# Performance work log

Hardware: AMD Instinct MI355X
Metric: run time of the kernel (lower is better)

## Reference

```python
import jax, jax.numpy as jnp
import numpy as np

NC = 10   # num_classes
H = 6     # num_heads
C = 384   # dim
HD = C // H
B = 16    # batch (non-anchor rows)
T = 197   # tokens (1 cls + 196 image)
N = T - 1
SCALE = HD ** -0.5


def _ln(x, g, b):
    mu = jnp.mean(x, -1, keepdims=True)
    var = jnp.mean(jnp.square(x - mu), -1, keepdims=True)
    return (x - mu) * jax.lax.rsqrt(var + 1e-5) * g + b


def setup_inputs() -> dict:
    key = jax.random.key(0)
    ks = jax.random.split(key, 12)
    def w(k, shape):
        return jax.random.normal(k, shape, jnp.float32) * 0.02
    return {
        "x": jax.random.normal(ks[0], (B + NC, T, C), jnp.float32),
        "Wqv": w(ks[1], (C, 2 * C)),
        "Wk": w(ks[2], (C, C)),
        "Wq_proj": w(ks[3], (C, C)), "bq_proj": jnp.zeros((C,), jnp.float32),
        "Wqk": w(ks[4], (C, C)), "Wqk2": w(ks[5], (C, C)), "Wv": w(ks[6], (C, C)),
        "Wr_proj": w(ks[7], (C, C)), "br_proj": jnp.zeros((C,), jnp.float32),
        "g1": jnp.ones((C,), jnp.float32), "b1": jnp.zeros((C,), jnp.float32),
        "g2": jnp.ones((C,), jnp.float32), "b2": jnp.zeros((C,), jnp.float32),
        "g3": jnp.ones((C,), jnp.float32), "b3": jnp.zeros((C,), jnp.float32),
        "W1": w(ks[8], (C, 4 * C)), "bm1": jnp.zeros((4 * C,), jnp.float32),
        "W2": w(ks[9], (4 * C, C)), "bm2": jnp.zeros((C,), jnp.float32),
    }


def reference(x, Wqv, Wk, Wq_proj, bq_proj, Wqk, Wqk2, Wv, Wr_proj, br_proj,
              g1, b1, g2, b2, g3, b3, W1, bm1, W2, bm2):
    xs, anchors = x[:-NC], jax.lax.stop_gradient(x[-NC:])  # anchors .detach()
    x_im, a_im = xs[:, 1:], anchors[:, 1:]                  # [B,N,C], [NC,N,C]
    x_cls, a_cls = xs[:, :1], anchors[:, :1]                # [B,1,C], [NC,1,C]

    # ---- Quoter ----
    n1x = _ln(x_cls, g1, b1)[:, 0]    # [B,C]
    n1a = _ln(a_cls, g1, b1)[:, 0]    # [NC,C]
    qv = (n1a @ Wqv).reshape(NC, 2, H, HD)
    q, v = qv[:, 0], qv[:, 1]                       # [NC,H,HD]
    k = (n1x @ Wk).reshape(B, H, HD)                # [B,H,HD]
    attn_cls = jax.nn.softmax(jnp.einsum('nhd,bhd->bnh', q, k) * SCALE, axis=1)  # [B,NC,H]
    cls_out = jnp.einsum('bnh,nhd->bhd', attn_cls, v).reshape(B, 1, C) @ Wq_proj + bq_proj

    # ---- Rectifier ----
    n2x = _ln(x_im, g2, b2)   # [B,N,C]
    n2a = _ln(a_im, g2, b2)   # [NC,N,C]
    def heads(t, W):
        return (t @ W).reshape(t.shape[0], N, H, HD).transpose(0, 2, 1, 3)
    vr = heads(n2x, Wv)        # [B,H,N,HD]
    qh = heads(n2x, Wqk)       # [B,H,N,HD]
    kh = heads(n2a, Wqk)       # [NC,H,N,HD]
    q2 = heads(n2x, Wqk2)
    k2 = heads(n2a, Wqk2)
    # left_attn = relu(-(q @ k^T) * scale), right_attn = relu((k2 @ q2^T) * scale)
    left = jax.nn.relu(-SCALE * jnp.einsum('bhnd,chmd->bchnm', qh, kh))    # [B,NC,H,N,N]
    right = jax.nn.relu(SCALE * jnp.einsum('chmd,bhnd->bchmn', k2, q2))    # [B,NC,H,N,N]
    attn = jnp.einsum('bchnm,bchmk->bchnk', left, right).transpose(0, 2, 3, 1, 4)  # [B,H,N,NC,N]
    # faithful raw reshape [B,NC,H] -> [B,H,NC] (memory reinterpretation as in torch source)
    w2 = attn_cls.reshape(B, H, NC)
    tmp = jnp.einsum('bhc,bhnck->bhnk', w2, attn)                           # [B,H,N,N]
    # faithful raw reshape [B,H,N,HD] -> [B,N,C]
    rect = jnp.einsum('bhnk,bhkd->bhnd', tmp, vr).reshape(B, N, C) @ Wr_proj + br_proj

    x_im = x_im + rect
    xx = jnp.concatenate([cls_out, x_im], axis=1)        # [B,T,C]
    hdn = _ln(xx, g3, b3)
    xx = xx + (jax.nn.gelu(hdn @ W1 + bm1, approximate=False) @ W2 + bm2)
    return jnp.concatenate([xx, anchors], axis=0)        # [B+NC,T,C]
```

## Files before the change

### kernel.cpp

```cpp
#include <hip/hip_runtime.h>
#include <hip/hip_bf16.h>
#include <math.h>

#define SCL 0.125f

typedef float f32x4 __attribute__((ext_vector_type(4)));
typedef short bf16x8 __attribute__((ext_vector_type(8)));
#define MFMA16(a, b, c) __builtin_amdgcn_mfma_f32_16x16x32_bf16((a), (b), (c), 0, 0, 0)

__device__ __forceinline__ unsigned short f2bf(float f) {
    unsigned int u = __builtin_bit_cast(unsigned int, f);
    u = (u + 0x7FFFu + ((u >> 16) & 1u)) >> 16;
    return (unsigned short)u;
}

__device__ __forceinline__ float gelu_exact(float v) {
    return 0.5f * v * (1.f + erff(v * 0.70710678118654752f));
}

template <int BF16OUT>
__global__ void ln_kernel(const float* __restrict__ x, void* __restrict__ outp,
                          const float* __restrict__ g, const float* __restrict__ bt,
                          int mode) {
    const int row = blockIdx.x;
    const int lane = threadIdx.x;
    const float* src;
    if (mode == 0)      src = x + (size_t)row * (197 * 384);
    else if (mode == 1) { int b = row / 196, n = row % 196; src = x + (size_t)(b * 197 + 1 + n) * 384; }
    else if (mode == 2) { int b = row / 196, n = row % 196; src = x + (size_t)((16 + b) * 197 + 1 + n) * 384; }
    else                src = x + (size_t)row * 384;

    float v[6];
    float s = 0.f, s2 = 0.f;
#pragma unroll
    for (int j = 0; j < 6; j++) {
        v[j] = src[lane + j * 64];
        s += v[j];
        s2 += v[j] * v[j];
    }
#pragma unroll
    for (int o = 32; o; o >>= 1) {
        s  += __shfl_xor(s, o);
        s2 += __shfl_xor(s2, o);
    }
    const float mu = s * (1.f / 384.f);
    const float var = s2 * (1.f / 384.f) - mu * mu;
    const float rs = 1.f / sqrtf(var + 1e-5f);
#pragma unroll
    for (int j = 0; j < 6; j++) {
        const int c = lane + j * 64;
        const float r = (v[j] - mu) * rs * g[c] + bt[c];
        if (BF16OUT) ((unsigned short*)outp)[(size_t)row * 384 + c] = f2bf(r);
        else         ((float*)outp)[(size_t)row * 384 + c] = r;
    }
}

template <int M>
__global__ void gemm_cls(const float* __restrict__ A, const float* __restrict__ B,
                         const float* __restrict__ bias, float* __restrict__ C,
                         int N, int ldc) {
    __shared__ float sA[M * 384];
    __shared__ float red[4][M][64];
    const int t = threadIdx.x;
    const int tc = t & 63, ks = t >> 6;
    const int n = blockIdx.x * 64 + tc;
    for (int e = t; e < M * 384; e += 256) sA[e] = A[e];
    __syncthreads();
    float acc[M];
#pragma unroll
    for (int m = 0; m < M; m++) acc[m] = 0.f;
    const int k0 = ks * 96;
#pragma unroll 4
    for (int k = k0; k < k0 + 96; k++) {
        const float bv = B[(size_t)k * N + n];
#pragma unroll
        for (int m = 0; m < M; m++) acc[m] += sA[m * 384 + k] * bv;
    }
#pragma unroll
    for (int m = 0; m < M; m++) red[ks][m][tc] = acc[m];
    __syncthreads();
    if (ks == 0) {
#pragma unroll
        for (int m = 0; m < M; m++) {
            float s = red[0][m][tc] + red[1][m][tc] + red[2][m][tc] + red[3][m][tc];
            if (bias) s += bias[n];
            C[(size_t)m * ldc + n] = s;
        }
    }
}

__global__ void attn_cls_kernel(const float* __restrict__ qv, const float* __restrict__ kcls,
                                float* __restrict__ aflat, float* __restrict__ cls_pre) {
    const int b = blockIdx.x;
    const int t = threadIdx.x;
    __shared__ float kb[384];
    __shared__ float pl[60];
#pragma unroll
    for (int j = 0; j < 6; j++) kb[t + j * 64] = kcls[b * 384 + t + j * 64];
    __syncthreads();
    if (t < 60) {
        const int n = t / 6, h = t % 6;
        float acc = 0.f;
        for (int d = 0; d < 64; d++) acc += qv[n * 768 + h * 64 + d] * kb[h * 64 + d];
        pl[t] = acc * SCL;
    }
    __syncthreads();
    if (t < 6) {
        float m = -1e30f;
        for (int n = 0; n < 10; n++) m = fmaxf(m, pl[n * 6 + t]);
        float p[10], sum = 0.f;
        for (int n = 0; n < 10; n++) { p[n] = expf(pl[n * 6 + t] - m); sum += p[n]; }
        const float inv = 1.f / sum;
        for (int n = 0; n < 10; n++) {
            const float pr = p[n] * inv;
            pl[n * 6 + t] = pr;
            aflat[b * 60 + n * 6 + t] = pr;
        }
    }
    __syncthreads();
#pragma unroll
    for (int j = 0; j < 6; j++) {
        const int c = t + j * 64;
        const int h = c >> 6;
        float acc = 0.f;
        for (int n = 0; n < 10; n++) acc += pl[n * 6 + h] * qv[n * 768 + 384 + c];
        cls_pre[b * 384 + c] = acc;
    }
}

__global__ void wcast_t(const float* __restrict__ W, unsigned short* __restrict__ Wt,
                        int K, int N) {
    const int n0 = blockIdx.x * 64, k0 = blockIdx.y * 64;
    __shared__ unsigned short sT[64][72];
    const int t = threadIdx.x;
    for (int e = t; e < 4096; e += 256) {
        const int k = e >> 6, n = e & 63;
        sT[n][k] = f2bf(W[(size_t)(k0 + k) * N + n0 + n]);
    }
    __syncthreads();
    for (int e = t; e < 512; e += 256) {
        const int n = e >> 3, ch = e & 7;
        *(uint4*)&Wt[(size_t)(n0 + n) * K + k0 + ch * 8] = *(uint4*)&sT[n][ch * 8];
    }
}

__global__ void wcast3(const float* __restrict__ Wa, const float* __restrict__ Wb,
                       const float* __restrict__ Wc, unsigned short* __restrict__ Wt) {
    const float* W = blockIdx.z == 0 ? Wa : (blockIdx.z == 1 ? Wb : Wc);
    unsigned short* dst = Wt + (size_t)blockIdx.z * 384 * 384;
    const int n0 = blockIdx.x * 64, k0 = blockIdx.y * 64;
    __shared__ unsigned short sT[64][72];
    const int t = threadIdx.x;
    for (int e = t; e < 4096; e += 256) {
        const int k = e >> 6, n = e & 63;
        sT[n][k] = f2bf(W[(size_t)(k0 + k) * 384 + n0 + n]);
    }
    __syncthreads();
    for (int e = t; e < 512; e += 256) {
        const int n = e >> 3, ch = e & 7;
        *(uint4*)&dst[(size_t)(n0 + n) * 384 + k0 + ch * 8] = *(uint4*)&sT[n][ch * 8];
    }
}

template <int EPI>
__launch_bounds__(256)
__global__ void gemm_mfma(const unsigned short* __restrict__ A,
                          const unsigned short* __restrict__ Bt,
                          const float* __restrict__ bias, const float* __restrict__ res,
                          void* __restrict__ Cout, int M, int N, int K) {
    const int m0 = blockIdx.y * 64, n0 = blockIdx.x * 128;
    const int t = threadIdx.x;
    const int w = t >> 6, l = t & 63;
    const int lr = l & 15, lk = l >> 4;
    const int wr = w >> 1, wc = w & 1;

    __shared__ unsigned short sA[64][72];
    __shared__ unsigned short sB[128][72];

    f32x4 acc[2][4];
#pragma unroll
    for (int mi = 0; mi < 2; mi++)
#pragma unroll
        for (int nj = 0; nj < 4; nj++) acc[mi][nj] = (f32x4){0.f, 0.f, 0.f, 0.f};

    for (int k0 = 0; k0 < K; k0 += 64) {
        for (int e = t; e < 512; e += 256) {
            const int r = e >> 3, ch = e & 7;
            uint4 v = make_uint4(0, 0, 0, 0);
            const int row = m0 + r;
            if (row < M) v = *(const uint4*)(A + (size_t)row * K + k0 + ch * 8);
            *(uint4*)&sA[r][ch * 8] = v;
        }
        for (int e = t; e < 1024; e += 256) {
            const int r = e >> 3, ch = e & 7;
            *(uint4*)&sB[r][ch * 8] = *(const uint4*)(Bt + (size_t)(n0 + r) * K + k0 + ch * 8);
        }
        __syncthreads();
#pragma unroll
        for (int kc = 0; kc < 2; kc++) {
            bf16x8 af[2], bfr[4];
#pragma unroll
            for (int mi = 0; mi < 2; mi++)
                af[mi] = *(const bf16x8*)&sA[wr * 32 + mi * 16 + lr][kc * 32 + lk * 8];
#pragma unroll
            for (int nj = 0; nj < 4; nj++)
                bfr[nj] = *(const bf16x8*)&sB[wc * 64 + nj * 16 + lr][kc * 32 + lk * 8];
#pragma unroll
            for (int mi = 0; mi < 2; mi++)
#pragma unroll
                for (int nj = 0; nj < 4; nj++)
                    acc[mi][nj] = MFMA16(af[mi], bfr[nj], acc[mi][nj]);
        }
        __syncthreads();
    }

#pragma unroll
    for (int mi = 0; mi < 2; mi++)
#pragma unroll
        for (int nj = 0; nj < 4; nj++) {
            const int col = n0 + wc * 64 + nj * 16 + lr;
#pragma unroll
            for (int i = 0; i < 4; i++) {
                const int row = m0 + wr * 32 + mi * 16 + lk * 4 + i;
                if (row >= M) continue;
                float v = acc[mi][nj][i];
                if (EPI == 0) {
                    ((unsigned short*)Cout)[(size_t)row * N + col] = f2bf(v);
                } else if (EPI == 1) {
                    const int crow = row + row / 196 + 1;
                    v += bias[col] + res[(size_t)crow * N + col];
                    ((float*)Cout)[(size_t)crow * N + col] = v;
                } else if (EPI == 2) {
                    ((unsigned short*)Cout)[(size_t)row * N + col] = f2bf(gelu_exact(v + bias[col]));
                } else {
                    v += bias[col] + res[(size_t)row * N + col];
                    ((float*)Cout)[(size_t)row * N + col] = v;
                }
            }
        }
}

__global__ __launch_bounds__(256, 1)
void rz_kernel(const unsigned short* __restrict__ Q2b, const unsigned short* __restrict__ K2b,
               const unsigned short* __restrict__ VRb, unsigned short* __restrict__ Zt,
               int sq, int sk, int sv) {
    const int c = blockIdx.x, h = blockIdx.y, b = blockIdx.z;
    const int t = threadIdx.x;
    const int w = t >> 6, l = t & 63;
    const int lr = l & 15;
    const int lk = l >> 4;

    __shared__ unsigned short sm[78208];
    unsigned short* sQ2 = sm;
    unsigned short* sVT = sm;
    unsigned short* sK2 = sm + 14976;
    unsigned short* sR  = sm + 29952;

    const unsigned short* q2src = Q2b + (size_t)(b * 196) * sq + h * 64;
    const unsigned short* k2src = K2b + (size_t)(c * 196) * sk + h * 64;
    for (int e = t; e < 208 * 8; e += 256) {
        const int r = e >> 3, ch = e & 7;
        uint4 v = make_uint4(0, 0, 0, 0);
        if (r < 196) v = *(const uint4*)(q2src + (size_t)r * sq + ch * 8);
        *(uint4*)&sQ2[r * 72 + ch * 8] = v;
    }
    for (int e = t; e < 208 * 8; e += 256) {
        const int r = e >> 3, ch = e & 7;
        uint4 v = make_uint4(0, 0, 0, 0);
        if (r < 196) v = *(const uint4*)(k2src + (size_t)r * sk + ch * 8);
        *(uint4*)&sK2[r * 72 + ch * 8] = v;
    }
    for (int e = t; e < 208 * 16; e += 256) sR[(e >> 4) * 232 + 208 + (e & 15)] = 0;
    __syncthreads();

    for (int tt = w; tt < 169; tt += 4) {
        const int mt = tt / 13, kt = tt % 13;
        f32x4 acc = {0.f, 0.f, 0.f, 0.f};
        bf16x8 a0 = *(const bf16x8*)&sK2[(mt * 16 + lr) * 72 + lk * 8];
        bf16x8 b0 = *(const bf16x8*)&sQ2[(kt * 16 + lr) * 72 + lk * 8];
        acc = MFMA16(a0, b0, acc);
        bf16x8 a1 = *(const bf16x8*)&sK2[(mt * 16 + lr) * 72 + 32 + lk * 8];
        bf16x8 b1 = *(const bf16x8*)&sQ2[(kt * 16 + lr) * 72 + 32 + lk * 8];
        acc = MFMA16(a1, b1, acc);
        const int rrow = mt * 16 + lk * 4, rcol = kt * 16 + lr;
#pragma unroll
        for (int i = 0; i < 4; i++)
            sR[(rrow + i) * 232 + rcol] = f2bf(fmaxf(0.f, SCL * acc[i]));
    }
    __syncthreads();

    const unsigned short* vrsrc = VRb + (size_t)(b * 196) * sv + h * 64;
    for (int e = t; e < 196 * 8; e += 256) {
        const int kk = e >> 3, ch = e & 7;
        uint4 v = *(const uint4*)(vrsrc + (size_t)kk * sv + ch * 8);
        unsigned short vs[8]; *(uint4*)vs = v;
#pragma unroll
        for (int j = 0; j < 8; j++) sVT[(ch * 8 + j) * 232 + kk] = vs[j];
    }
    for (int e = t; e < 64 * 36; e += 256) sVT[(e / 36) * 232 + 196 + (e % 36)] = 0;
    __syncthreads();

    unsigned short* zdst = Zt + ((((size_t)(b * 6 + h)) * 10 + c) * 64) * 208;
    for (int tt = w; tt < 52; tt += 4) {
        const int mt = tt >> 2, dt = tt & 3;
        f32x4 acc = {0.f, 0.f, 0.f, 0.f};
#pragma unroll
        for (int kc = 0; kc < 7; kc++) {
            bf16x8 a = *(const bf16x8*)&sR[(mt * 16 + lr) * 232 + kc * 32 + lk * 8];
            bf16x8 bb = *(const bf16x8*)&sVT[(dt * 16 + lr) * 232 + kc * 32 + lk * 8];
            acc = MFMA16(a, bb, acc);
        }
        unsigned short p[4];
#pragma unroll
        for (int i = 0; i < 4; i++) p[i] = f2bf(acc[i]);
        *(uint2*)&zdst[(size_t)(dt * 16 + lr) * 208 + mt * 16 + lk * 4] = *(uint2*)p;
    }
}

__global__ __launch_bounds__(256)
void yz_kernel(const unsigned short* __restrict__ QHb, const unsigned short* __restrict__ KHb,
               const unsigned short* __restrict__ Zt, const float* __restrict__ aflat,
               unsigned short* __restrict__ rect) {
    const int ns = blockIdx.x, h = blockIdx.y, b = blockIdx.z;
    const int n0 = ns * 49;
    const int t = threadIdx.x;
    const int w = t >> 6, l = t & 63;
    const int lr = l & 15, lk = l >> 4;

    __shared__ unsigned short sKH[112 * 72];
    __shared__ unsigned short sZT[64 * 232];
    __shared__ unsigned short sL[64 * 232];

    for (int e = t; e < 64 * 24; e += 256) {
        sZT[(e / 24) * 232 + 208 + (e % 24)] = 0;
        sL [(e / 24) * 232 + 208 + (e % 24)] = 0;
    }

    bf16x8 qf[2];
    {
        const int rel = w * 16 + lr;
        if (rel < 49) {
            const unsigned short* qsrc = QHb + (size_t)(b * 196 + n0 + rel) * 1152 + h * 64;
            qf[0] = *(const bf16x8*)(qsrc + lk * 8);
            qf[1] = *(const bf16x8*)(qsrc + 32 + lk * 8);
        } else {
            qf[0] = (bf16x8){0, 0, 0, 0, 0, 0, 0, 0};
            qf[1] = (bf16x8){0, 0, 0, 0, 0, 0, 0, 0};
        }
    }

    f32x4 y[4];
#pragma unroll
    for (int i = 0; i < 4; i++) y[i] = (f32x4){0.f, 0.f, 0.f, 0.f};
    __syncthreads();

    for (int c = 0; c < 10; c++) {
        const unsigned short* zsrc = Zt + ((((size_t)(b * 6 + h)) * 10 + c) * 64) * 208;
        for (int e = t; e < 64 * 26; e += 256) {
            const int d = e / 26, mc = e % 26;
            *(uint4*)&sZT[d * 232 + mc * 8] = *(const uint4*)(zsrc + (size_t)d * 208 + mc * 8);
        }
        for (int e = t; e < 112 * 8; e += 256) {
            const int r = e >> 3, ch = e & 7;
            *(uint4*)&sKH[r * 72 + ch * 8] =
                *(const uint4*)(KHb + (size_t)(c * 196 + r) * 768 + h * 64 + ch * 8);
        }
        const float wc = aflat[b * 60 + h * 10 + c];
        __syncthreads();
#pragma unroll
        for (int mt = 0; mt < 7; mt++) {
            f32x4 acc = {0.f, 0.f, 0.f, 0.f};
            bf16x8 b0 = *(const bf16x8*)&sKH[(mt * 16 + lr) * 72 + lk * 8];
            acc = MFMA16(qf[0], b0, acc);
            bf16x8 b1 = *(const bf16x8*)&sKH[(mt * 16 + lr) * 72 + 32 + lk * 8];
            acc = MFMA16(qf[1], b1, acc);
            const int lrow = w * 16 + lk * 4, lcol = mt * 16 + lr;
#pragma unroll
            for (int i = 0; i < 4; i++)
                sL[(lrow + i) * 232 + lcol] = f2bf(wc * fmaxf(0.f, -SCL * acc[i]));
        }
        __syncthreads();
        for (int e = t; e < 96 * 8; e += 256) {
            const int r = e >> 3, ch = e & 7;
            uint4 v = make_uint4(0, 0, 0, 0);
            if (112 + r < 196)
                v = *(const uint4*)(KHb + (size_t)(c * 196 + 112 + r) * 768 + h * 64 + ch * 8);
            *(uint4*)&sKH[r * 72 + ch * 8] = v;
        }
        __syncthreads();
#pragma unroll
        for (int mt = 7; mt < 13; mt++) {
            f32x4 acc = {0.f, 0.f, 0.f, 0.f};
            bf16x8 b0 = *(const bf16x8*)&sKH[((mt - 7) * 16 + lr) * 72 + lk * 8];
            acc = MFMA16(qf[0], b0, acc);
            bf16x8 b1 = *(const bf16x8*)&sKH[((mt - 7) * 16 + lr) * 72 + 32 + lk * 8];
            acc = MFMA16(qf[1], b1, acc);
            const int lrow = w * 16 + lk * 4, lcol = mt * 16 + lr;
#pragma unroll
            for (int i = 0; i < 4; i++)
                sL[(lrow + i) * 232 + lcol] = f2bf(wc * fmaxf(0.f, -SCL * acc[i]));
        }
#pragma unroll
        for (int dt = 0; dt < 4; dt++) {
            f32x4 acc = y[dt];
#pragma unroll
            for (int mc = 0; mc < 7; mc++) {
                bf16x8 a  = *(const bf16x8*)&sL[(w * 16 + lr) * 232 + mc * 32 + lk * 8];
                bf16x8 bb = *(const bf16x8*)&sZT[(dt * 16 + lr) * 232 + mc * 32 + lk * 8];
                acc = MFMA16(a, bb, acc);
            }
            y[dt] = acc;
        }
        __syncthreads();
    }

#pragma unroll
    for (int dt = 0; dt < 4; dt++)
#pragma unroll
        for (int i = 0; i < 4; i++) {
            const int rel = w * 16 + lk * 4 + i;
            if (rel < 49)
                rect[(((size_t)(b * 6 + h)) * 196 + n0 + rel) * 64 + dt * 16 + lr] = f2bf(y[dt][i]);
        }
}

__global__ void copy_anchors(const float* __restrict__ x, float* __restrict__ out) {
    const int e = blockIdx.x * 256 + threadIdx.x;
    if (e < 189120) {
        const int base = 16 * 197 * 384 / 4;
        ((float4*)out)[base + e] = ((const float4*)x)[base + e];
    }
}

extern "C" void kernel_launch(void* const* d_in, const int* in_sizes, int n_in,
                              void* d_out, int out_size, void* d_ws, size_t ws_size,
                              hipStream_t stream) {
    (void)in_sizes; (void)n_in; (void)out_size; (void)ws_size;
    const float* x       = (const float*)d_in[0];
    const float* Wqv     = (const float*)d_in[1];
    const float* Wk      = (const float*)d_in[2];
    const float* Wq_proj = (const float*)d_in[3];
    const float* bq_proj = (const float*)d_in[4];
    const float* Wqk     = (const float*)d_in[5];
    const float* Wqk2    = (const float*)d_in[6];
    const float* Wv      = (const float*)d_in[7];
    const float* Wr_proj = (const float*)d_in[8];
    const float* br_proj = (const float*)d_in[9];
    const float* g1      = (const float*)d_in[10];
    const float* b1      = (const float*)d_in[11];
    const float* g2      = (const float*)d_in[12];
    const float* b2      = (const float*)d_in[13];
    const float* g3      = (const float*)d_in[14];
    const float* b3      = (const float*)d_in[15];
    const float* W1      = (const float*)d_in[16];
    const float* bm1     = (const float*)d_in[17];
    const float* W2      = (const float*)d_in[18];
    const float* bm2     = (const float*)d_in[19];

    float* ws = (float*)d_ws;
    float* n1      = ws;
    float* qv      = ws + 9984;
    float* kcls    = ws + 17664;
    float* aflat   = ws + 23808;
    float* cls_pre = ws + 24768;
    unsigned short* n2x_bf  = (unsigned short*)(ws + 30912);
    unsigned short* n2a_bf  = (unsigned short*)(ws + 633024);
    unsigned short* Px      = (unsigned short*)(ws + 1009344);
    unsigned short* Pa      = (unsigned short*)(ws + 2815680);
    unsigned short* rect_bf = (unsigned short*)(ws + 3568320);
    float* xx               = ws + 4170432;
    unsigned short* Wx_t    = (unsigned short*)(ws + 5380800);
    unsigned short* Wr_t    = (unsigned short*)(ws + 5601984);
    unsigned short* W1_t    = (unsigned short*)(ws + 5675712);
    unsigned short* W2_t    = (unsigned short*)(ws + 5970624);
    unsigned short* Zt      = (unsigned short*)(ws + 6265536);
    unsigned short* hdn_bf  = (unsigned short*)(ws + 6265536);
    unsigned short* G_bf    = (unsigned short*)(ws + 6870720);
    float* outf = (float*)d_out;

    unsigned short* QHb = Px;
    unsigned short* Q2b = Px + 384;
    unsigned short* VRb = Px + 768;
    unsigned short* KHb = Pa;
    unsigned short* K2b = Pa + 384;

    wcast3<<<dim3(6, 6, 3), 256, 0, stream>>>(Wqk, Wqk2, Wv, Wx_t);
    wcast_t<<<dim3(6, 6),  256, 0, stream>>>(Wr_proj, Wr_t, 384, 384);
    wcast_t<<<dim3(24, 6), 256, 0, stream>>>(W1, W1_t, 384, 1536);
    wcast_t<<<dim3(6, 24), 256, 0, stream>>>(W2, W2_t, 1536, 384);
    ln_kernel<0><<<26, 64, 0, stream>>>(x, n1, g1, b1, 0);
    gemm_cls<10><<<12, 256, 0, stream>>>(n1 + 16 * 384, Wqv, nullptr, qv, 768, 768);
    gemm_cls<16><<<6, 256, 0, stream>>>(n1, Wk, nullptr, kcls, 384, 384);
    attn_cls_kernel<<<16, 64, 0, stream>>>(qv, kcls, aflat, cls_pre);
    ln_kernel<1><<<3136, 64, 0, stream>>>(x, n2x_bf, g2, b2, 1);
    ln_kernel<1><<<1960, 64, 0, stream>>>(x, n2a_bf, g2, b2, 2);
    gemm_mfma<0><<<dim3(9, 49), 256, 0, stream>>>(n2x_bf, Wx_t, nullptr, nullptr, Px, 3136, 1152, 384);
    gemm_mfma<0><<<dim3(6, 31), 256, 0, stream>>>(n2a_bf, Wx_t, nullptr, nullptr, Pa, 1960, 768, 384);
    rz_kernel<<<dim3(10, 6, 16), 256, 0, stream>>>(Q2b, K2b, VRb, Zt, 1152, 768, 1152);
    yz_kernel<<<dim3(4, 6, 16), 256, 0, stream>>>(QHb, KHb, Zt, aflat, rect_bf);
    gemm_cls<16><<<6, 256, 0, stream>>>(cls_pre, Wq_proj, bq_proj, xx, 384, 197 * 384);
    gemm_mfma<1><<<dim3(3, 49), 256, 0, stream>>>(rect_bf, Wr_t, br_proj, x, xx, 3136, 384, 384);
    ln_kernel<1><<<3152, 64, 0, stream>>>(xx, hdn_bf, g3, b3, 3);
    gemm_mfma<2><<<dim3(12, 50), 256, 0, stream>>>(hdn_bf, W1_t, bm1, nullptr, G_bf, 3152, 1536, 384);
    gemm_mfma<3><<<dim3(3, 50), 256, 0, stream>>>(G_bf, W2_t, bm2, xx, outf, 3152, 384, 1536);
    copy_anchors<<<739, 256, 0, stream>>>(x, outf);
}
```

Baseline: 503.4 us.

## Restructure rz_kernel to hold Q2 fragments in registers and fuse per-wave strips

rz_kernel now keeps all Q2 MFMA fragments in registers and loads K2 rows directly from global memory. Each wave computes a 16-row strip of relu(K2·Q2ᵀ) into its own LDS buffer and immediately multiplies it by Vᵀ. This shrinks shared memory use enough to allow two blocks per CU and removes the full-tile staging and a barrier. Separately, the two image-token LayerNorm launches (x and anchors) are merged into one launch, which relies on the anchor output buffer sitting directly after the x buffer. The risk is higher register pressure from 26 held fragments.

```diff
diff --git a/kernel.cpp b/kernel.cpp
--- a/kernel.cpp
+++ b/kernel.cpp
@@ -26,8 +26,10 @@
     const int lane = threadIdx.x;
     const float* src;
     if (mode == 0)      src = x + (size_t)row * (197 * 384);
-    else if (mode == 1) { int b = row / 196, n = row % 196; src = x + (size_t)(b * 197 + 1 + n) * 384; }
-    else if (mode == 2) { int b = row / 196, n = row % 196; src = x + (size_t)((16 + b) * 197 + 1 + n) * 384; }
+    else if (mode == 4) {
+        if (row < 3136) { int b = row / 196, n = row % 196; src = x + (size_t)(b * 197 + 1 + n) * 384; }
+        else { int rr = row - 3136; int b = rr / 196, n = rr % 196; src = x + (size_t)((16 + b) * 197 + 1 + n) * 384; }
+    }
     else                src = x + (size_t)row * 384;
 
     float v[6];
@@ -240,54 +242,18 @@
         }
 }
 
-__global__ __launch_bounds__(256, 1)
+__global__ __launch_bounds__(256, 2)
 void rz_kernel(const unsigned short* __restrict__ Q2b, const unsigned short* __restrict__ K2b,
                const unsigned short* __restrict__ VRb, unsigned short* __restrict__ Zt,
                int sq, int sk, int sv) {
     const int c = blockIdx.x, h = blockIdx.y, b = blockIdx.z;
     const int t = threadIdx.x;
     const int w = t >> 6, l = t & 63;
-    const int lr = l & 15;
-    const int lk = l >> 4;
-
-    __shared__ unsigned short sm[78208];
-    unsigned short* sQ2 = sm;
-    unsigned short* sVT = sm;
-    unsigned short* sK2 = sm + 14976;
-    unsigned short* sR  = sm + 29952;
-
-    const unsigned short* q2src = Q2b + (size_t)(b * 196) * sq + h * 64;
-    const unsigned short* k2src = K2b + (size_t)(c * 196) * sk + h * 64;
-    for (int e = t; e < 208 * 8; e += 256) {
-        const int r = e >> 3, ch = e & 7;
-        uint4 v = make_uint4(0, 0, 0, 0);
-        if (r < 196) v = *(const uint4*)(q2src + (size_t)r * sq + ch * 8);
-        *(uint4*)&sQ2[r * 72 + ch * 8] = v;
-    }
-    for (int e = t; e < 208 * 8; e += 256) {
-        const int r = e >> 3, ch = e & 7;
-        uint4 v = make_uint4(0, 0, 0, 0);
-        if (r < 196) v = *(const uint4*)(k2src + (size_t)r * sk + ch * 8);
-        *(uint4*)&sK2[r * 72 + ch * 8] = v;
-    }
-    for (int e = t; e < 208 * 16; e += 256) sR[(e >> 4) * 232 + 208 + (e & 15)] = 0;
-    __syncthreads();
-
-    for (int tt = w; tt < 169; tt += 4) {
-        const int mt = tt / 13, kt = tt % 13;
-        f32x4 acc = {0.f, 0.f, 0.f, 0.f};
-        bf16x8 a0 = *(const bf16x8*)&sK2[(mt * 16 + lr) * 72 + lk * 8];
-        bf16x8 b0 = *(const bf16x8*)&sQ2[(kt * 16 + lr) * 72 + lk * 8];
-        acc = MFMA16(a0, b0, acc);
-        bf16x8 a1 = *(const bf16x8*)&sK2[(mt * 16 + lr) * 72 + 32 + lk * 8];
-        bf16x8 b1 = *(const bf16x8*)&sQ2[(kt * 16 + lr) * 72 + 32 + lk * 8];
-        acc = MFMA16(a1, b1, acc);
-        const int rrow = mt * 16 + lk * 4, rcol = kt * 16 + lr;
-#pragma unroll
-        for (int i = 0; i < 4; i++)
-            sR[(rrow + i) * 232 + rcol] = f2bf(fmaxf(0.f, SCL * acc[i]));
-    }
-    __syncthreads();
+    const int lr = l & 15, lk = l >> 4;
+
+    __shared__ unsigned short sVT[64 * 232];
+    __shared__ unsigned short sR[4 * 16 * 232];
+    unsigned short* sRw = sR + w * (16 * 232);
 
     const unsigned short* vrsrc = VRb + (size_t)(b * 196) * sv + h * 64;
     for (int e = t; e < 196 * 8; e += 256) {
@@ -298,22 +264,61 @@
         for (int j = 0; j < 8; j++) sVT[(ch * 8 + j) * 232 + kk] = vs[j];
     }
     for (int e = t; e < 64 * 36; e += 256) sVT[(e / 36) * 232 + 196 + (e % 36)] = 0;
-    __syncthreads();
-
+    for (int e = l; e < 16 * 24; e += 64) sRw[(e / 24) * 232 + 208 + (e % 24)] = 0;
+
+    bf16x8 qf0[13], qf1[13];
+    const unsigned short* q2src = Q2b + (size_t)(b * 196) * sq + h * 64;
+#pragma unroll
+    for (int kt = 0; kt < 13; kt++) {
+        const int r = kt * 16 + lr;
+        if (r < 196) {
+            const unsigned short* p = q2src + (size_t)r * sq;
+            qf0[kt] = *(const bf16x8*)(p + lk * 8);
+            qf1[kt] = *(const bf16x8*)(p + 32 + lk * 8);
+        } else {
+            qf0[kt] = (bf16x8){0, 0, 0, 0, 0, 0, 0, 0};
+            qf1[kt] = (bf16x8){0, 0, 0, 0, 0, 0, 0, 0};
+        }
+    }
+    __syncthreads();
+
+    const unsigned short* k2src = K2b + (size_t)(c * 196) * sk + h * 64;
     unsigned short* zdst = Zt + ((((size_t)(b * 6 + h)) * 10 + c) * 64) * 208;
-    for (int tt = w; tt < 52; tt += 4) {
-        const int mt = tt >> 2, dt = tt & 3;
-        f32x4 acc = {0.f, 0.f, 0.f, 0.f};
-#pragma unroll
-        for (int kc = 0; kc < 7; kc++) {
-            bf16x8 a = *(const bf16x8*)&sR[(mt * 16 + lr) * 232 + kc * 32 + lk * 8];
-            bf16x8 bb = *(const bf16x8*)&sVT[(dt * 16 + lr) * 232 + kc * 32 + lk * 8];
-            acc = MFMA16(a, bb, acc);
-        }
-        unsigned short p[4];
-#pragma unroll
-        for (int i = 0; i < 4; i++) p[i] = f2bf(acc[i]);
-        *(uint2*)&zdst[(size_t)(dt * 16 + lr) * 208 + mt * 16 + lk * 4] = *(uint2*)p;
+
+    for (int mt = w; mt < 13; mt += 4) {
+        bf16x8 a0, a1;
+        const int ar = mt * 16 + lr;
+        if (ar < 196) {
+            const unsigned short* p = k2src + (size_t)ar * sk;
+            a0 = *(const bf16x8*)(p + lk * 8);
+            a1 = *(const bf16x8*)(p + 32 + lk * 8);
+        } else {
+            a0 = (bf16x8){0, 0, 0, 0, 0, 0, 0, 0};
+            a1 = (bf16x8){0, 0, 0, 0, 0, 0, 0, 0};
+        }
+#pragma unroll
+        for (int kt = 0; kt < 13; kt++) {
+            f32x4 acc = {0.f, 0.f, 0.f, 0.f};
+            acc = MFMA16(a0, qf0[kt], acc);
+            acc = MFMA16(a1, qf1[kt], acc);
+#pragma unroll
+            for (int i = 0; i < 4; i++)
+                sRw[(lk * 4 + i) * 232 + kt * 16 + lr] = f2bf(fmaxf(0.f, SCL * acc[i]));
+        }
+#pragma unroll
+        for (int dt = 0; dt < 4; dt++) {
+            f32x4 acc = {0.f, 0.f, 0.f, 0.f};
+#pragma unroll
+            for (int kc = 0; kc < 7; kc++) {
+                bf16x8 a  = *(const bf16x8*)&sRw[lr * 232 + kc * 32 + lk * 8];
+                bf16x8 bb = *(const bf16x8*)&sVT[(dt * 16 + lr) * 232 + kc * 32 + lk * 8];
+                acc = MFMA16(a, bb, acc);
+            }
+            unsigned short p[4];
+#pragma unroll
+            for (int i = 0; i < 4; i++) p[i] = f2bf(acc[i]);
+            *(uint2*)&zdst[(size_t)(dt * 16 + lr) * 208 + mt * 16 + lk * 4] = *(uint2*)p;
+        }
     }
 }
 
@@ -492,8 +497,7 @@
     gemm_cls<10><<<12, 256, 0, stream>>>(n1 + 16 * 384, Wqv, nullptr, qv, 768, 768);
     gemm_cls<16><<<6, 256, 0, stream>>>(n1, Wk, nullptr, kcls, 384, 384);
     attn_cls_kernel<<<16, 64, 0, stream>>>(qv, kcls, aflat, cls_pre);
-    ln_kernel<1><<<3136, 64, 0, stream>>>(x, n2x_bf, g2, b2, 1);
-    ln_kernel<1><<<1960, 64, 0, stream>>>(x, n2a_bf, g2, b2, 2);
+    ln_kernel<1><<<5096, 64, 0, stream>>>(x, n2x_bf, g2, b2, 4);
     gemm_mfma<0><<<dim3(9, 49), 256, 0, stream>>>(n2x_bf, Wx_t, nullptr, nullptr, Px, 3136, 1152, 384);
     gemm_mfma<0><<<dim3(6, 31), 256, 0, stream>>>(n2a_bf, Wx_t, nullptr, nullptr, Pa, 1960, 768, 384);
     rz_kernel<<<dim3(10, 6, 16), 256, 0, stream>>>(Q2b, K2b, VRb, Zt, 1152, 768, 1152);
```

New measurement: 470.1 us. -6.6%, faster.
